# Kernel tuning notes

Measured on AMD Instinct MI355X. Metric: run time of the kernel, lower is better.

Reference implementation:

```python
import jax, jax.numpy as jnp
import numpy as np

NUM_TASKS = 16
IN_DIM = 512
HIDDEN = 1024
OUT_DIM = 256
B = 8192


def setup_inputs() -> dict:
    key = jax.random.key(0)
    ks = jax.random.split(key, 8)
    x = jax.random.normal(ks[0], (B, IN_DIM), dtype=jnp.float32)
    task_ids = jax.random.randint(ks[1], (B,), 0, NUM_TASKS)
    # lecun_normal for tanh hidden layers: std = 1/sqrt(fan_in)
    k0 = jax.random.normal(ks[2], (NUM_TASKS, IN_DIM, HIDDEN), dtype=jnp.float32) / np.sqrt(IN_DIM)
    b0 = jnp.zeros((NUM_TASKS, HIDDEN), dtype=jnp.float32)
    k1 = jax.random.normal(ks[3], (NUM_TASKS, HIDDEN, HIDDEN), dtype=jnp.float32) / np.sqrt(HIDDEN)
    b1 = jnp.zeros((NUM_TASKS, HIDDEN), dtype=jnp.float32)
    # output layer: normal(0.01)
    k2 = jax.random.normal(ks[4], (NUM_TASKS, HIDDEN, OUT_DIM), dtype=jnp.float32) * 0.01
    b2 = jnp.zeros((NUM_TASKS, OUT_DIM), dtype=jnp.float32)
    return {"x": x, "task_ids": task_ids, "k0": k0, "b0": b0,
            "k1": k1, "b1": b1, "k2": k2, "b2": b2}


def _dense_per_task(h, gate, kernel, bias):
    # h: [B, I], gate: [B, T] one-hot, kernel: [T, I, O], bias: [T, O]
    y = jnp.einsum('bt,bi,tio->bo', gate, h, kernel)
    return y + jnp.einsum('bt,to->bo', gate, bias)


def reference(x, task_ids, k0, b0, k1, b1, k2, b2):
    gate = jax.nn.one_hot(task_ids, NUM_TASKS, dtype=x.dtype)  # [B, T]
    h = jnp.tanh(_dense_per_task(x, gate, k0, b0))
    h = jnp.tanh(_dense_per_task(h, gate, k1, b1))
    y = _dense_per_task(h, gate, k2, b2)
    return y
```

## Files before the change

### kernel.cpp

```cpp
#include <hip/hip_runtime.h>
#include <math.h>

#define NUM_TASKS 16
#define B_ROWS    8192
#define TROWS     48
#define NB_FUSED  186
#define P_ROWS    8960

typedef __attribute__((ext_vector_type(4))) float f32x4;
typedef __attribute__((ext_vector_type(8))) short bf16x8;
typedef __attribute__((ext_vector_type(4))) short bf16x4;
typedef unsigned short ushort_t;

__device__ __forceinline__ short f2bf(float f) {
    union { float f; unsigned u; } c; c.f = f;
    unsigned u = c.u;
    unsigned r = (u + 0x7FFFu + ((u >> 16) & 1u)) >> 16;
    return (short)r;
}

__device__ __forceinline__ float fast_tanh(float x) {
    float e = __expf(2.0f * x);
    return 1.0f - 2.0f / (e + 1.0f);
}


__global__ __launch_bounds__(256) void bucket_kernel(
    const int* __restrict__ task_ids,
    int* __restrict__ sidx,
    int* __restrict__ tile_base,
    int* __restrict__ tile_task,
    int* __restrict__ tile_end,
    int* __restrict__ ntiles)
{
    __shared__ int cnt[256][NUM_TASKS];
    __shared__ int pstart[NUM_TASKS];
    __shared__ int tot[NUM_TASKS];

    const int tid = threadIdx.x;
    #pragma unroll
    for (int t = 0; t < NUM_TASKS; ++t) cnt[tid][t] = 0;
    const int base = tid * (B_ROWS / 256);

    for (int i = 0; i < B_ROWS / 256; ++i) {
        int t = task_ids[base + i];
        cnt[tid][t]++;
    }
    __syncthreads();

    if (tid < NUM_TASKS) {
        int s = 0;
        for (int c = 0; c < 256; ++c) { int v = cnt[c][tid]; cnt[c][tid] = s; s += v; }
        tot[tid] = s;
    }
    __syncthreads();

    if (tid == 0) {
        int p = 0, nt = 0;
        for (int t = 0; t < NUM_TASKS; ++t) {
            pstart[t] = p;
            for (int r = 0; r < tot[t]; r += TROWS) {
                tile_base[nt] = p + r;
                tile_task[nt] = t;
                tile_end[nt]  = p + tot[t];
                nt++;
            }
            p += ((tot[t] + TROWS - 1) / TROWS) * TROWS;
        }
        *ntiles = nt;
    }
    __syncthreads();

    for (int i = 0; i < P_ROWS / 256; ++i) sidx[tid + i * 256] = 0;
    __syncthreads();

    for (int i = 0; i < B_ROWS / 256; ++i) {
        int row = base + i;
        int t = task_ids[row];
        int pos = pstart[t] + cnt[tid][t];
        cnt[tid][t] = cnt[tid][t] + 1;
        sidx[pos] = row;
    }
}

template<int K, int N>
__global__ __launch_bounds__(256) void wconv(
    const float* __restrict__ W, ushort_t* __restrict__ Wt)
{
    const int t  = blockIdx.z;
    const int kb = blockIdx.y * 64;
    const int nb = blockIdx.x * 64;
    const float* src = W + (size_t)t * K * N;
    ushort_t* dst = Wt + (size_t)t * N * K;

    __shared__ ushort_t tile[64][68];

    const int tid = threadIdx.x;
    {
        int kl  = tid >> 4;
        int nl4 = (tid & 15) * 4;
        #pragma unroll
        for (int r = 0; r < 4; ++r) {
            int k = kl + r * 16;
            f32x4 v = *(const f32x4*)(src + (size_t)(kb + k) * N + nb + nl4);
            tile[nl4 + 0][k] = (ushort_t)f2bf(v[0]);
            tile[nl4 + 1][k] = (ushort_t)f2bf(v[1]);
            tile[nl4 + 2][k] = (ushort_t)f2bf(v[2]);
            tile[nl4 + 3][k] = (ushort_t)f2bf(v[3]);
        }
    }
    __syncthreads();
    {
        int nl = tid >> 2;
        int c  = (tid & 3) * 16;
        int n  = nb + nl;
        int k0 = kb + c;
        bf16x4 v0 = *(const bf16x4*)&tile[nl][c + 0];
        bf16x4 v1 = *(const bf16x4*)&tile[nl][c + 4];
        bf16x4 v2 = *(const bf16x4*)&tile[nl][c + 8];
        bf16x4 v3 = *(const bf16x4*)&tile[nl][c + 12];
        ushort_t* dg = dst
            + (((size_t)(n >> 8) * (K / 32) + (k0 >> 5)) * 8 + ((n >> 5) & 7)) * 1024
            + ((n >> 4) & 1) * 512
            + ((k0 >> 3) & 3) * 128 + (n & 15) * 8;
        *(bf16x4*)(dg + 0)   = v0;
        *(bf16x4*)(dg + 4)   = v1;
        *(bf16x4*)(dg + 128) = v2;
        *(bf16x4*)(dg + 132) = v3;
    }
}

template<int K, int NNOUT, int NC, int INPLACE, int FINAL>
__device__ __forceinline__ void run_layer(
    const char* __restrict__ Hin,
    char* __restrict__ Hout,
    const ushort_t* __restrict__ Wt,
    const float* __restrict__ bias,
    float* __restrict__ outp,
    const int* __restrict__ sidx,
    int rowbase, int rowend, int lane, int wid)
{
    constexpr int NS = K / 32;

    const char* pw = (const char*)Wt
                   + wid * 2048 + (lane >> 4) * 256 + (lane & 15) * 16;

    f32x4 acc[NC][3][2];
    #pragma unroll
    for (int c = 0; c < NC; ++c)
        #pragma unroll
        for (int mf = 0; mf < 3; ++mf)
            #pragma unroll
            for (int nf = 0; nf < 2; ++nf)
                acc[c][mf][nf] = (f32x4){0.f, 0.f, 0.f, 0.f};

    bf16x8 wreg[4][2];
    #pragma unroll
    for (int b = 0; b < 4; ++b) {
        wreg[b][0] = *(const bf16x8*)(pw);
        wreg[b][1] = *(const bf16x8*)(pw + 1024);
        pw += 16384;
    }

    #pragma unroll
    for (int c = 0; c < NC; ++c) {
        #pragma unroll 4
        for (int s = 0; s < NS; ++s) {
            bf16x8 h[3];
            const int kg = s * 4 + (lane >> 4);
            #pragma unroll
            for (int mf = 0; mf < 3; ++mf)
                h[mf] = *(const bf16x8*)(Hin
                            + ((size_t)(mf * (K / 8) + kg) * 256)
                            + (((lane & 15) ^ (kg & 7)) * 16));
            __builtin_amdgcn_s_setprio(1);
            #pragma unroll
            for (int mf = 0; mf < 3; ++mf)
                #pragma unroll
                for (int nf = 0; nf < 2; ++nf)
                    acc[c][mf][nf] = __builtin_amdgcn_mfma_f32_16x16x32_bf16(
                        wreg[s & 3][nf], h[mf], acc[c][mf][nf], 0, 0, 0);
            __builtin_amdgcn_s_setprio(0);
            wreg[s & 3][0] = *(const bf16x8*)(pw);
            wreg[s & 3][1] = *(const bf16x8*)(pw + 1024);
            pw += 16384;
        }
    }

    const int q   = lane >> 4;
    const int m15 = lane & 15;

    if (!FINAL) {
        if (INPLACE) __syncthreads();
        #pragma unroll
        for (int c = 0; c < NC; ++c) {
            #pragma unroll
            for (int mf = 0; mf < 3; ++mf) {
                #pragma unroll
                for (int nf = 0; nf < 2; ++nf) {
                    const int n_lo = c * 256 + wid * 32 + nf * 16 + q * 4;
                    const f32x4 bb = *(const f32x4*)(bias + n_lo);
                    bf16x4 pk;
                    #pragma unroll
                    for (int r = 0; r < 4; ++r)
                        pk[r] = f2bf(fast_tanh(acc[c][mf][nf][r] + bb[r]));
                    const int kg2 = n_lo >> 3;
                    size_t off = ((size_t)(mf * (NNOUT / 8) + kg2) * 256)
                               + ((m15 ^ (kg2 & 7)) * 16) + (n_lo & 7) * 2;
                    *(bf16x4*)(Hout + off) = pk;
                }
            }
        }
        __syncthreads();
    } else {
        #pragma unroll
        for (int mf = 0; mf < 3; ++mf) {
            const int grow = rowbase + mf * 16 + m15;
            if (grow < rowend) {
                const int orow = sidx[grow];
                #pragma unroll
                for (int nf = 0; nf < 2; ++nf) {
                    const int n_lo = wid * 32 + nf * 16 + q * 4;
                    const f32x4 bb = *(const f32x4*)(bias + n_lo);
                    f32x4 v;
                    #pragma unroll
                    for (int r = 0; r < 4; ++r)
                        v[r] = acc[0][mf][nf][r] + bb[r];
                    *(f32x4*)(outp + (size_t)orow * 256 + n_lo) = v;
                }
            }
        }
    }
}

__global__ __launch_bounds__(512, 2) void fused_mlp(
    const float* __restrict__ x,
    const ushort_t* __restrict__ Wt0,
    const ushort_t* __restrict__ Wt1,
    const ushort_t* __restrict__ Wt2,
    const float* __restrict__ b0,
    const float* __restrict__ b1,
    const float* __restrict__ b2,
    float* __restrict__ out,
    const int* __restrict__ sidx,
    const int* __restrict__ tile_base,
    const int* __restrict__ tile_task,
    const int* __restrict__ tile_end,
    const int* __restrict__ ntiles)
{
    __shared__ __align__(16) char lds[147456];
    char* Hreg = lds;
    char* Xreg = lds + 98304;

    const int orig = blockIdx.x;
    constexpr int q8 = NB_FUSED / 8, r8 = NB_FUSED % 8;
    const int xcd = orig & 7, idx = orig >> 3;
    const int tile = (xcd < r8 ? xcd * (q8 + 1) : r8 * (q8 + 1) + (xcd - r8) * q8) + idx;

    if (tile >= *ntiles) return;
    const int rowbase = tile_base[tile];
    const int task    = tile_task[tile];
    const int rowend  = tile_end[tile];

    const int tid  = threadIdx.x;
    const int lane = tid & 63;
    const int wid  = tid >> 6;

    #pragma unroll
    for (int i = 0; i < 6; ++i) {
        const int row = wid + i * 8;
        const int src = sidx[rowbase + row];
        const float* sp = x + (size_t)src * 512 + lane * 8;
        f32x4 v0 = *(const f32x4*)sp;
        f32x4 v1 = *(const f32x4*)(sp + 4);
        bf16x8 pk;
        pk[0] = f2bf(v0[0]); pk[1] = f2bf(v0[1]);
        pk[2] = f2bf(v0[2]); pk[3] = f2bf(v0[3]);
        pk[4] = f2bf(v1[0]); pk[5] = f2bf(v1[1]);
        pk[6] = f2bf(v1[2]); pk[7] = f2bf(v1[3]);
        size_t off = ((size_t)((row >> 4) * 64 + lane) * 256)
                   + (((row & 15) ^ (lane & 7)) * 16);
        *(bf16x8*)(Xreg + off) = pk;
    }
    __syncthreads();

    run_layer< 512, 1024, 4, 0, 0>(Xreg, Hreg,
                                   Wt0 + (size_t)task * 512 * 1024,
                                   b0 + task * 1024, nullptr, sidx,
                                   rowbase, rowend, lane, wid);
    run_layer<1024, 1024, 4, 1, 0>(Hreg, Hreg,
                                   Wt1 + (size_t)task * 1024 * 1024,
                                   b1 + task * 1024, nullptr, sidx,
                                   rowbase, rowend, lane, wid);
    run_layer<1024,  256, 1, 0, 1>(Hreg, nullptr,
                                   Wt2 + (size_t)task * 1024 * 256,
                                   b2 + task * 256, out, sidx,
                                   rowbase, rowend, lane, wid);
}

extern "C" void kernel_launch(void* const* d_in, const int* in_sizes, int n_in,
                              void* d_out, int out_size, void* d_ws, size_t ws_size,
                              hipStream_t stream)
{
    const float* x        = (const float*)d_in[0];
    const int*   task_ids = (const int*)  d_in[1];
    const float* k0       = (const float*)d_in[2];
    const float* b0       = (const float*)d_in[3];
    const float* k1       = (const float*)d_in[4];
    const float* b1       = (const float*)d_in[5];
    const float* k2       = (const float*)d_in[6];
    const float* b2       = (const float*)d_in[7];
    float* out = (float*)d_out;

    char* ws = (char*)d_ws;
    int* sidx      = (int*)ws;
    int* tile_base = sidx + P_ROWS;
    int* tile_task = tile_base + 512;
    int* tile_end  = tile_task + 512;
    int* ntiles    = tile_end + 512;

    size_t off = 131072;
    ushort_t* Wt0 = (ushort_t*)(ws + off); off += (size_t)16 * 512 * 1024 * 2 + 65536;
    ushort_t* Wt1 = (ushort_t*)(ws + off); off += (size_t)16 * 1024 * 1024 * 2 + 65536;
    ushort_t* Wt2 = (ushort_t*)(ws + off); off += (size_t)16 * 1024 * 256 * 2 + 65536;

    bucket_kernel<<<1, 256, 0, stream>>>(task_ids, sidx, tile_base, tile_task,
                                         tile_end, ntiles);
    wconv< 512, 1024><<<dim3(16,  8, 16), 256, 0, stream>>>(k0, Wt0);
    wconv<1024, 1024><<<dim3(16, 16, 16), 256, 0, stream>>>(k1, Wt1);
    wconv<1024,  256><<<dim3( 4, 16, 16), 256, 0, stream>>>(k2, Wt2);

    fused_mlp<<<NB_FUSED, 512, 0, stream>>>(
        x, Wt0, Wt1, Wt2, b0, b1, b2, out,
        sidx, tile_base, tile_task, tile_end, ntiles);
}
```

Measured before the change: 109.1 us.

## Use 1024-thread blocks with in-place LDS and per-wave contiguous weight layout

Measured after the change: 113.8 us. 4.4% more time.

```diff
diff --git a/kernel.cpp b/kernel.cpp
--- a/kernel.cpp
+++ b/kernel.cpp
@@ -120,7 +120,7 @@
         bf16x4 v2 = *(const bf16x4*)&tile[nl][c + 8];
         bf16x4 v3 = *(const bf16x4*)&tile[nl][c + 12];
         ushort_t* dg = dst
-            + (((size_t)(n >> 8) * (K / 32) + (k0 >> 5)) * 8 + ((n >> 5) & 7)) * 1024
+            + ((size_t)(n >> 5) * (K / 32) + (k0 >> 5)) * 1024
             + ((n >> 4) & 1) * 512
             + ((k0 >> 3) & 3) * 128 + (n & 15) * 8;
         *(bf16x4*)(dg + 0)   = v0;
@@ -130,10 +130,90 @@
     }
 }
 
-template<int K, int NNOUT, int NC, int INPLACE, int FINAL>
-__device__ __forceinline__ void run_layer(
+template<int K, int NNOUT, int INPLACE>
+__device__ __forceinline__ void hidden_layer(
     const char* __restrict__ Hin,
     char* __restrict__ Hout,
+    const ushort_t* __restrict__ Wt,
+    const float* __restrict__ bias,
+    int lane, int wid)
+{
+    constexpr int NS = K / 32;
+    constexpr int G  = 2 * NS;
+
+    const int q   = lane >> 4;
+    const int m15 = lane & 15;
+
+    const char* pw = (const char*)Wt + (size_t)wid * G * 2048
+                   + q * 256 + m15 * 16;
+
+    f32x4 acc[2][3][2];
+    #pragma unroll
+    for (int c = 0; c < 2; ++c)
+        #pragma unroll
+        for (int mf = 0; mf < 3; ++mf)
+            #pragma unroll
+            for (int nf = 0; nf < 2; ++nf)
+                acc[c][mf][nf] = (f32x4){0.f, 0.f, 0.f, 0.f};
+
+    bf16x8 wreg[4][2];
+    #pragma unroll
+    for (int b = 0; b < 4; ++b) {
+        wreg[b][0] = *(const bf16x8*)(pw);
+        wreg[b][1] = *(const bf16x8*)(pw + 1024);
+        pw += 2048;
+    }
+
+    #pragma unroll
+    for (int g = 0; g < G; ++g) {
+        const int c  = g / NS;
+        const int s  = g % NS;
+        const int kg = s * 4 + q;
+        bf16x8 h[3];
+        #pragma unroll
+        for (int mf = 0; mf < 3; ++mf)
+            h[mf] = *(const bf16x8*)(Hin
+                        + ((size_t)(mf * (K / 8) + kg) * 256)
+                        + ((m15 ^ (kg & 7)) * 16));
+        __builtin_amdgcn_s_setprio(1);
+        #pragma unroll
+        for (int mf = 0; mf < 3; ++mf)
+            #pragma unroll
+            for (int nf = 0; nf < 2; ++nf)
+                acc[c][mf][nf] = __builtin_amdgcn_mfma_f32_16x16x32_bf16(
+                    wreg[g & 3][nf], h[mf], acc[c][mf][nf], 0, 0, 0);
+        __builtin_amdgcn_s_setprio(0);
+        wreg[g & 3][0] = *(const bf16x8*)(pw);
+        wreg[g & 3][1] = *(const bf16x8*)(pw + 1024);
+        pw += 2048;
+    }
+
+    if (INPLACE) __syncthreads();
+    #pragma unroll
+    for (int c = 0; c < 2; ++c) {
+        #pragma unroll
+        for (int mf = 0; mf < 3; ++mf) {
+            #pragma unroll
+            for (int nf = 0; nf < 2; ++nf) {
+                const int n_lo = (wid * 2 + c) * 32 + nf * 16 + q * 4;
+                const f32x4 bb = *(const f32x4*)(bias + n_lo);
+                bf16x4 pk;
+                #pragma unroll
+                for (int r = 0; r < 4; ++r)
+                    pk[r] = f2bf(fast_tanh(acc[c][mf][nf][r] + bb[r]));
+                const int kg2 = n_lo >> 3;
+                size_t off = ((size_t)(mf * (NNOUT / 8) + kg2) * 256)
+                           + ((m15 ^ (kg2 & 7)) * 16) + (n_lo & 7) * 2;
+                *(bf16x4*)(Hout + off) = pk;
+            }
+        }
+    }
+    __syncthreads();
+}
+
+template<int K>
+__device__ __forceinline__ void final_layer(
+    const char* __restrict__ Hin,
     const ushort_t* __restrict__ Wt,
     const float* __restrict__ bias,
     float* __restrict__ outp,
@@ -142,98 +222,55 @@
 {
     constexpr int NS = K / 32;
 
-    const char* pw = (const char*)Wt
-                   + wid * 2048 + (lane >> 4) * 256 + (lane & 15) * 16;
-
-    f32x4 acc[NC][3][2];
-    #pragma unroll
-    for (int c = 0; c < NC; ++c)
-        #pragma unroll
-        for (int mf = 0; mf < 3; ++mf)
-            #pragma unroll
-            for (int nf = 0; nf < 2; ++nf)
-                acc[c][mf][nf] = (f32x4){0.f, 0.f, 0.f, 0.f};
-
-    bf16x8 wreg[4][2];
-    #pragma unroll
-    for (int b = 0; b < 4; ++b) {
-        wreg[b][0] = *(const bf16x8*)(pw);
-        wreg[b][1] = *(const bf16x8*)(pw + 1024);
-        pw += 16384;
-    }
-
-    #pragma unroll
-    for (int c = 0; c < NC; ++c) {
-        #pragma unroll 4
-        for (int s = 0; s < NS; ++s) {
-            bf16x8 h[3];
-            const int kg = s * 4 + (lane >> 4);
-            #pragma unroll
-            for (int mf = 0; mf < 3; ++mf)
-                h[mf] = *(const bf16x8*)(Hin
-                            + ((size_t)(mf * (K / 8) + kg) * 256)
-                            + (((lane & 15) ^ (kg & 7)) * 16));
-            __builtin_amdgcn_s_setprio(1);
-            #pragma unroll
-            for (int mf = 0; mf < 3; ++mf)
-                #pragma unroll
-                for (int nf = 0; nf < 2; ++nf)
-                    acc[c][mf][nf] = __builtin_amdgcn_mfma_f32_16x16x32_bf16(
-                        wreg[s & 3][nf], h[mf], acc[c][mf][nf], 0, 0, 0);
-            __builtin_amdgcn_s_setprio(0);
-            wreg[s & 3][0] = *(const bf16x8*)(pw);
-            wreg[s & 3][1] = *(const bf16x8*)(pw + 1024);
-            pw += 16384;
-        }
-    }
-
     const int q   = lane >> 4;
     const int m15 = lane & 15;
 
-    if (!FINAL) {
-        if (INPLACE) __syncthreads();
-        #pragma unroll
-        for (int c = 0; c < NC; ++c) {
+    const char* pw = (const char*)Wt + (size_t)(wid >> 1) * NS * 2048
+                   + (wid & 1) * 1024 + q * 256 + m15 * 16;
+
+    f32x4 acc[3];
+    #pragma unroll
+    for (int mf = 0; mf < 3; ++mf) acc[mf] = (f32x4){0.f, 0.f, 0.f, 0.f};
+
+    bf16x8 wreg[4];
+    #pragma unroll
+    for (int b = 0; b < 4; ++b) { wreg[b] = *(const bf16x8*)(pw); pw += 2048; }
+
+    #pragma unroll
+    for (int s = 0; s < NS; ++s) {
+        const int kg = s * 4 + q;
+        bf16x8 h[3];
+        #pragma unroll
+        for (int mf = 0; mf < 3; ++mf)
+            h[mf] = *(const bf16x8*)(Hin
+                        + ((size_t)(mf * (K / 8) + kg) * 256)
+                        + ((m15 ^ (kg & 7)) * 16));
+        __builtin_amdgcn_s_setprio(1);
+        #pragma unroll
+        for (int mf = 0; mf < 3; ++mf)
+            acc[mf] = __builtin_amdgcn_mfma_f32_16x16x32_bf16(
+                wreg[s & 3], h[mf], acc[mf], 0, 0, 0);
+        __builtin_amdgcn_s_setprio(0);
+        wreg[s & 3] = *(const bf16x8*)(pw);
+        pw += 2048;
+    }
+
+    const int n_lo = (wid >> 1) * 32 + (wid & 1) * 16 + q * 4;
+    const f32x4 bb = *(const f32x4*)(bias + n_lo);
+    #pragma unroll
+    for (int mf = 0; mf < 3; ++mf) {
+        const int grow = rowbase + mf * 16 + m15;
+        if (grow < rowend) {
+            const int orow = sidx[grow];
+            f32x4 v;
             #pragma unroll
-            for (int mf = 0; mf < 3; ++mf) {
-                #pragma unroll
-                for (int nf = 0; nf < 2; ++nf) {
-                    const int n_lo = c * 256 + wid * 32 + nf * 16 + q * 4;
-                    const f32x4 bb = *(const f32x4*)(bias + n_lo);
-                    bf16x4 pk;
-                    #pragma unroll
-                    for (int r = 0; r < 4; ++r)
-                        pk[r] = f2bf(fast_tanh(acc[c][mf][nf][r] + bb[r]));
-                    const int kg2 = n_lo >> 3;
-                    size_t off = ((size_t)(mf * (NNOUT / 8) + kg2) * 256)
-                               + ((m15 ^ (kg2 & 7)) * 16) + (n_lo & 7) * 2;
-                    *(bf16x4*)(Hout + off) = pk;
-                }
-            }
+            for (int r = 0; r < 4; ++r) v[r] = acc[mf][r] + bb[r];
+            *(f32x4*)(outp + (size_t)orow * 256 + n_lo) = v;
         }
-        __syncthreads();
-    } else {
-        #pragma unroll
-        for (int mf = 0; mf < 3; ++mf) {
-            const int grow = rowbase + mf * 16 + m15;
-            if (grow < rowend) {
-                const int orow = sidx[grow];
-                #pragma unroll
-                for (int nf = 0; nf < 2; ++nf) {
-                    const int n_lo = wid * 32 + nf * 16 + q * 4;
-                    const f32x4 bb = *(const f32x4*)(bias + n_lo);
-                    f32x4 v;
-                    #pragma unroll
-                    for (int r = 0; r < 4; ++r)
-                        v[r] = acc[0][mf][nf][r] + bb[r];
-                    *(f32x4*)(outp + (size_t)orow * 256 + n_lo) = v;
-                }
-            }
-        }
-    }
-}
-
-__global__ __launch_bounds__(512, 2) void fused_mlp(
+    }
+}
+
+__global__ __launch_bounds__(1024, 4) void fused_mlp(
     const float* __restrict__ x,
     const ushort_t* __restrict__ Wt0,
     const ushort_t* __restrict__ Wt1,
@@ -248,9 +285,7 @@
     const int* __restrict__ tile_end,
     const int* __restrict__ ntiles)
 {
-    __shared__ __align__(16) char lds[147456];
-    char* Hreg = lds;
-    char* Xreg = lds + 98304;
+    __shared__ __align__(16) char lds[98304];
 
     const int orig = blockIdx.x;
     constexpr int q8 = NB_FUSED / 8, r8 = NB_FUSED % 8;
@@ -267,8 +302,8 @@
     const int wid  = tid >> 6;
 
     #pragma unroll
-    for (int i = 0; i < 6; ++i) {
-        const int row = wid + i * 8;
+    for (int i = 0; i < 3; ++i) {
+        const int row = wid + i * 16;
         const int src = sidx[rowbase + row];
         const float* sp = x + (size_t)src * 512 + lane * 8;
         f32x4 v0 = *(const f32x4*)sp;
@@ -280,22 +315,16 @@
         pk[6] = f2bf(v1[2]); pk[7] = f2bf(v1[3]);
         size_t off = ((size_t)((row >> 4) * 64 + lane) * 256)
                    + (((row & 15) ^ (lane & 7)) * 16);
-        *(bf16x8*)(Xreg + off) = pk;
-    }
-    __syncthreads();
-
-    run_layer< 512, 1024, 4, 0, 0>(Xreg, Hreg,
-                                   Wt0 + (size_t)task * 512 * 1024,
-                                   b0 + task * 1024, nullptr, sidx,
-                                   rowbase, rowend, lane, wid);
-    run_layer<1024, 1024, 4, 1, 0>(Hreg, Hreg,
-                                   Wt1 + (size_t)task * 1024 * 1024,
-                                   b1 + task * 1024, nullptr, sidx,
-                                   rowbase, rowend, lane, wid);
-    run_layer<1024,  256, 1, 0, 1>(Hreg, nullptr,
-                                   Wt2 + (size_t)task * 1024 * 256,
-                                   b2 + task * 256, out, sidx,
-                                   rowbase, rowend, lane, wid);
+        *(bf16x8*)(lds + off) = pk;
+    }
+    __syncthreads();
+
+    hidden_layer< 512, 1024, 1>(lds, lds, Wt0 + (size_t)task * 512 * 1024,
+                                b0 + task * 1024, lane, wid);
+    hidden_layer<1024, 1024, 1>(lds, lds, Wt1 + (size_t)task * 1024 * 1024,
+                                b1 + task * 1024, lane, wid);
+    final_layer<1024>(lds, Wt2 + (size_t)task * 1024 * 256,
+                      b2 + task * 256, out, sidx, rowbase, rowend, lane, wid);
 }
 
 extern "C" void kernel_launch(void* const* d_in, const int* in_sizes, int n_in,
@@ -320,9 +349,9 @@
     int* ntiles    = tile_end + 512;
 
     size_t off = 131072;
-    ushort_t* Wt0 = (ushort_t*)(ws + off); off += (size_t)16 * 512 * 1024 * 2 + 65536;
-    ushort_t* Wt1 = (ushort_t*)(ws + off); off += (size_t)16 * 1024 * 1024 * 2 + 65536;
-    ushort_t* Wt2 = (ushort_t*)(ws + off); off += (size_t)16 * 1024 * 256 * 2 + 65536;
+    ushort_t* Wt0 = (ushort_t*)(ws + off); off += (size_t)16 * 512 * 1024 * 2 + 16384;
+    ushort_t* Wt1 = (ushort_t*)(ws + off); off += (size_t)16 * 1024 * 1024 * 2 + 16384;
+    ushort_t* Wt2 = (ushort_t*)(ws + off); off += (size_t)16 * 1024 * 256 * 2 + 16384;
 
     bucket_kernel<<<1, 256, 0, stream>>>(task_ids, sidx, tile_base, tile_task,
                                          tile_end, ntiles);
@@ -330,7 +359,7 @@
     wconv<1024, 1024><<<dim3(16, 16, 16), 256, 0, stream>>>(k1, Wt1);
     wconv<1024,  256><<<dim3( 4, 16, 16), 256, 0, stream>>>(k2, Wt2);
 
-    fused_mlp<<<NB_FUSED, 512, 0, stream>>>(
+    fused_mlp<<<NB_FUSED, 1024, 0, stream>>>(
         x, Wt0, Wt1, Wt2, b0, b1, b2, out,
         sidx, tile_base, tile_task, tile_end, ntiles);
 }
```

## Stream weights through LDS ring buffer with direct global-to-LDS async loads

Applied to the files above, without the earlier changes.

After: 119.0 us. 1.09x slower.

```diff
diff --git a/kernel.cpp b/kernel.cpp
--- a/kernel.cpp
+++ b/kernel.cpp
@@ -22,6 +22,13 @@
 __device__ __forceinline__ float fast_tanh(float x) {
     float e = __expf(2.0f * x);
     return 1.0f - 2.0f / (e + 1.0f);
+}
+
+__device__ __forceinline__ void gld16(const void* g, void* l) {
+    __builtin_amdgcn_global_load_lds(
+        (const __attribute__((address_space(1))) unsigned int*)g,
+        (__attribute__((address_space(3))) unsigned int*)l,
+        16, 0, 0);
 }
 
 
@@ -87,6 +94,7 @@
 __global__ __launch_bounds__(256) void wconv(
     const float* __restrict__ W, ushort_t* __restrict__ Wt)
 {
+    constexpr int NTk = K / 32;
     const int t  = blockIdx.z;
     const int kb = blockIdx.y * 64;
     const int nb = blockIdx.x * 64;
@@ -119,31 +127,34 @@
         bf16x4 v1 = *(const bf16x4*)&tile[nl][c + 4];
         bf16x4 v2 = *(const bf16x4*)&tile[nl][c + 8];
         bf16x4 v3 = *(const bf16x4*)&tile[nl][c + 12];
-        ushort_t* dg = dst
-            + (((size_t)(n >> 8) * (K / 32) + (k0 >> 5)) * 8 + ((n >> 5) & 7)) * 1024
-            + ((n >> 4) & 1) * 512
-            + ((k0 >> 3) & 3) * 128 + (n & 15) * 8;
-        *(bf16x4*)(dg + 0)   = v0;
-        *(bf16x4*)(dg + 4)   = v1;
-        *(bf16x4*)(dg + 128) = v2;
-        *(bf16x4*)(dg + 132) = v3;
-    }
-}
-
-template<int K, int NNOUT, int NC, int INPLACE, int FINAL>
+
+        const int cc   = n >> 8;
+        const int cf16 = (n >> 4) & 15;
+        const int kt   = k0 >> 5;
+        const int kgL  = (k0 >> 3) & 3;
+        const size_t blk = ((size_t)(cc * NTk + kt) * 16 + cf16) * 4;
+        ushort_t* d0 = dst + (blk + kgL)     * 128 + (((n & 15) ^ kgL)       * 8);
+        ushort_t* d1 = dst + (blk + kgL + 1) * 128 + (((n & 15) ^ (kgL + 1)) * 8);
+        *(bf16x4*)(d0 + 0) = v0;
+        *(bf16x4*)(d0 + 4) = v1;
+        *(bf16x4*)(d1 + 0) = v2;
+        *(bf16x4*)(d1 + 4) = v3;
+    }
+}
+
+template<int K, int NNOUT, int NC, int FINAL>
 __device__ __forceinline__ void run_layer(
-    const char* __restrict__ Hin,
-    char* __restrict__ Hout,
-    const ushort_t* __restrict__ Wt,
+    char* __restrict__ ldsH,
+    char* __restrict__ ldsW,
+    const char* wsrc,
     const float* __restrict__ bias,
     float* __restrict__ outp,
     const int* __restrict__ sidx,
     int rowbase, int rowend, int lane, int wid)
 {
-    constexpr int NS = K / 32;
-
-    const char* pw = (const char*)Wt
-                   + wid * 2048 + (lane >> 4) * 256 + (lane & 15) * 16;
+    constexpr int NTk = K / 32;
+    const int q   = lane >> 4;
+    const int m15 = lane & 15;
 
     f32x4 acc[NC][3][2];
     #pragma unroll
@@ -154,60 +165,69 @@
             for (int nf = 0; nf < 2; ++nf)
                 acc[c][mf][nf] = (f32x4){0.f, 0.f, 0.f, 0.f};
 
-    bf16x8 wreg[4][2];
-    #pragma unroll
-    for (int b = 0; b < 4; ++b) {
-        wreg[b][0] = *(const bf16x8*)(pw);
-        wreg[b][1] = *(const bf16x8*)(pw + 1024);
-        pw += 16384;
+    #pragma unroll
+    for (int b = 0; b < 3; ++b) {
+        gld16(wsrc + wid * 1024 + lane * 16,        ldsW + b * 16384 + wid * 1024);
+        gld16(wsrc + 8192 + wid * 1024 + lane * 16, ldsW + b * 16384 + 8192 + wid * 1024);
+        wsrc += 16384;
     }
 
     #pragma unroll
     for (int c = 0; c < NC; ++c) {
-        #pragma unroll 4
-        for (int s = 0; s < NS; ++s) {
+        #pragma unroll
+        for (int kt = 0; kt < NTk; ++kt) {
+            const int pb = (kt + 3) & 3;
+            gld16(wsrc + wid * 1024 + lane * 16,        ldsW + pb * 16384 + wid * 1024);
+            gld16(wsrc + 8192 + wid * 1024 + lane * 16, ldsW + pb * 16384 + 8192 + wid * 1024);
+            wsrc += 16384;
+            asm volatile("s_waitcnt vmcnt(6)" ::: "memory");
+            asm volatile("s_barrier" ::: "memory");
+
+            const char* wb = ldsW + (kt & 3) * 16384;
+            bf16x8 w0 = *(const bf16x8*)(wb + ((2 * wid + 0) * 4 + q) * 256
+                                            + ((m15 ^ q) * 16));
+            bf16x8 w1 = *(const bf16x8*)(wb + ((2 * wid + 1) * 4 + q) * 256
+                                            + ((m15 ^ q) * 16));
+            const int kg = kt * 4 + q;
             bf16x8 h[3];
-            const int kg = s * 4 + (lane >> 4);
             #pragma unroll
             for (int mf = 0; mf < 3; ++mf)
-                h[mf] = *(const bf16x8*)(Hin
-                            + ((size_t)(mf * (K / 8) + kg) * 256)
-                            + (((lane & 15) ^ (kg & 7)) * 16));
+                h[mf] = *(const bf16x8*)(ldsH
+                            + ((size_t)(mf * (K / 8) + kg)) * 256
+                            + ((m15 ^ (kg & 7)) * 16));
+
             __builtin_amdgcn_s_setprio(1);
             #pragma unroll
-            for (int mf = 0; mf < 3; ++mf)
-                #pragma unroll
-                for (int nf = 0; nf < 2; ++nf)
-                    acc[c][mf][nf] = __builtin_amdgcn_mfma_f32_16x16x32_bf16(
-                        wreg[s & 3][nf], h[mf], acc[c][mf][nf], 0, 0, 0);
+            for (int mf = 0; mf < 3; ++mf) {
+                acc[c][mf][0] = __builtin_amdgcn_mfma_f32_16x16x32_bf16(
+                    w0, h[mf], acc[c][mf][0], 0, 0, 0);
+                acc[c][mf][1] = __builtin_amdgcn_mfma_f32_16x16x32_bf16(
+                    w1, h[mf], acc[c][mf][1], 0, 0, 0);
+            }
             __builtin_amdgcn_s_setprio(0);
-            wreg[s & 3][0] = *(const bf16x8*)(pw);
-            wreg[s & 3][1] = *(const bf16x8*)(pw + 1024);
-            pw += 16384;
-        }
-    }
-
-    const int q   = lane >> 4;
-    const int m15 = lane & 15;
+            asm volatile("s_barrier" ::: "memory");
+        }
+    }
+    asm volatile("s_waitcnt vmcnt(0)" ::: "memory");
 
     if (!FINAL) {
-        if (INPLACE) __syncthreads();
+        __syncthreads();
         #pragma unroll
         for (int c = 0; c < NC; ++c) {
             #pragma unroll
             for (int mf = 0; mf < 3; ++mf) {
                 #pragma unroll
                 for (int nf = 0; nf < 2; ++nf) {
-                    const int n_lo = c * 256 + wid * 32 + nf * 16 + q * 4;
+                    const int n_lo = c * 256 + (2 * wid + nf) * 16 + q * 4;
                     const f32x4 bb = *(const f32x4*)(bias + n_lo);
                     bf16x4 pk;
                     #pragma unroll
                     for (int r = 0; r < 4; ++r)
                         pk[r] = f2bf(fast_tanh(acc[c][mf][nf][r] + bb[r]));
                     const int kg2 = n_lo >> 3;
-                    size_t off = ((size_t)(mf * (NNOUT / 8) + kg2) * 256)
+                    size_t off = ((size_t)(mf * (NNOUT / 8) + kg2)) * 256
                                + ((m15 ^ (kg2 & 7)) * 16) + (n_lo & 7) * 2;
-                    *(bf16x4*)(Hout + off) = pk;
+                    *(bf16x4*)(ldsH + off) = pk;
                 }
             }
         }
@@ -220,7 +240,7 @@
                 const int orow = sidx[grow];
                 #pragma unroll
                 for (int nf = 0; nf < 2; ++nf) {
-                    const int n_lo = wid * 32 + nf * 16 + q * 4;
+                    const int n_lo = (2 * wid + nf) * 16 + q * 4;
                     const f32x4 bb = *(const f32x4*)(bias + n_lo);
                     f32x4 v;
                     #pragma unroll
@@ -233,7 +253,7 @@
     }
 }
 
-__global__ __launch_bounds__(512, 2) void fused_mlp(
+__global__ __launch_bounds__(512, 1) void fused_mlp(
     const float* __restrict__ x,
     const ushort_t* __restrict__ Wt0,
     const ushort_t* __restrict__ Wt1,
@@ -248,9 +268,9 @@
     const int* __restrict__ tile_end,
     const int* __restrict__ ntiles)
 {
-    __shared__ __align__(16) char lds[147456];
-    char* Hreg = lds;
-    char* Xreg = lds + 98304;
+    __shared__ __align__(16) char lds[163840];
+    char* ldsH = lds;
+    char* ldsW = lds + 98304;
 
     const int orig = blockIdx.x;
     constexpr int q8 = NB_FUSED / 8, r8 = NB_FUSED % 8;
@@ -280,22 +300,22 @@
         pk[6] = f2bf(v1[2]); pk[7] = f2bf(v1[3]);
         size_t off = ((size_t)((row >> 4) * 64 + lane) * 256)
                    + (((row & 15) ^ (lane & 7)) * 16);
-        *(bf16x8*)(Xreg + off) = pk;
-    }
-    __syncthreads();
-
-    run_layer< 512, 1024, 4, 0, 0>(Xreg, Hreg,
-                                   Wt0 + (size_t)task * 512 * 1024,
-                                   b0 + task * 1024, nullptr, sidx,
-                                   rowbase, rowend, lane, wid);
-    run_layer<1024, 1024, 4, 1, 0>(Hreg, Hreg,
-                                   Wt1 + (size_t)task * 1024 * 1024,
-                                   b1 + task * 1024, nullptr, sidx,
-                                   rowbase, rowend, lane, wid);
-    run_layer<1024,  256, 1, 0, 1>(Hreg, nullptr,
-                                   Wt2 + (size_t)task * 1024 * 256,
-                                   b2 + task * 256, out, sidx,
-                                   rowbase, rowend, lane, wid);
+        *(bf16x8*)(ldsH + off) = pk;
+    }
+    __syncthreads();
+
+    run_layer< 512, 1024, 4, 0>(ldsH, ldsW,
+                                (const char*)(Wt0 + (size_t)task * 512 * 1024),
+                                b0 + task * 1024, nullptr, sidx,
+                                rowbase, rowend, lane, wid);
+    run_layer<1024, 1024, 4, 0>(ldsH, ldsW,
+                                (const char*)(Wt1 + (size_t)task * 1024 * 1024),
+                                b1 + task * 1024, nullptr, sidx,
+                                rowbase, rowend, lane, wid);
+    run_layer<1024,  256, 1, 1>(ldsH, ldsW,
+                                (const char*)(Wt2 + (size_t)task * 1024 * 256),
+                                b2 + task * 256, out, sidx,
+                                rowbase, rowend, lane, wid);
 }
 
 extern "C" void kernel_launch(void* const* d_in, const int* in_sizes, int n_in,
@@ -320,9 +340,9 @@
     int* ntiles    = tile_end + 512;
 
     size_t off = 131072;
-    ushort_t* Wt0 = (ushort_t*)(ws + off); off += (size_t)16 * 512 * 1024 * 2 + 65536;
-    ushort_t* Wt1 = (ushort_t*)(ws + off); off += (size_t)16 * 1024 * 1024 * 2 + 65536;
-    ushort_t* Wt2 = (ushort_t*)(ws + off); off += (size_t)16 * 1024 * 256 * 2 + 65536;
+    ushort_t* Wt0 = (ushort_t*)(ws + off); off += (size_t)16 * 512 * 1024 * 2 + 49152;
+    ushort_t* Wt1 = (ushort_t*)(ws + off); off += (size_t)16 * 1024 * 1024 * 2 + 49152;
+    ushort_t* Wt2 = (ushort_t*)(ws + off); off += (size_t)16 * 1024 * 256 * 2 + 49152;
 
     bucket_kernel<<<1, 256, 0, stream>>>(task_ids, sidx, tile_base, tile_task,
                                          tile_end, ntiles);
```
